# Optimization experiments

Hardware: AMD Instinct MI355X
Metric: run time of the kernel (lower is better)

The kernel has to match this reference:

```python
import jax, jax.numpy as jnp
import numpy as np

B, T, H, C = 32, 2048, 200, 256

def conv1d(x, w):
    # x: [B, T, Cin], w: [K, Cin, Cout], padding SAME, stride 1
    return jax.lax.conv_general_dilated(x, w, (1,), 'SAME',
                                        dimension_numbers=('NWC', 'WIO', 'NWC'))

def reverse_sequence(x, lengths):
    # tf.reverse_sequence along time axis 1
    t = jnp.arange(x.shape[1])[None, :]          # [1, T]
    L = lengths[:, None]                          # [B, 1]
    idx = jnp.where(t < L, L - 1 - t, t)          # [B, T]
    return jnp.take_along_axis(x, idx[:, :, None], axis=1)

def lstm(x, lengths, W, b):
    # BasicLSTMCell: gates [i, j, f, o], forget_bias=1.0
    xT = jnp.transpose(x, (1, 0, 2))              # [T, B, C]
    c0 = jnp.zeros((x.shape[0], H), x.dtype)
    h0 = jnp.zeros((x.shape[0], H), x.dtype)
    def step(carry, inp):
        c, h = carry
        xt, t = inp
        z = jnp.concatenate([xt, h], -1) @ W + b  # [B, 4H]
        i, j, f, o = jnp.split(z, 4, axis=-1)
        c_new = c * jax.nn.sigmoid(f + 1.0) + jax.nn.sigmoid(i) * jnp.tanh(j)
        h_new = jnp.tanh(c_new) * jax.nn.sigmoid(o)
        m = (t < lengths)[:, None]
        c2 = jnp.where(m, c_new, c)
        h2 = jnp.where(m, h_new, h)
        out = jnp.where(m, h_new, jnp.zeros_like(h_new))
        return (c2, h2), out
    _, ys = jax.lax.scan(step, (c0, h0), (xT, jnp.arange(xT.shape[0])))
    return jnp.transpose(ys, (1, 0, 2))           # [B, T, H]

def setup_inputs() -> dict:
    key = jax.random.key(0)
    ks = jax.random.split(key, 12)
    s = lambda k, shape, fan_in: jax.random.normal(k, shape, jnp.float32) * (1.0 / np.sqrt(fan_in))
    return {
        'signals': jax.random.normal(ks[0], (B, T, 1), jnp.float32),
        'sig_length': jax.random.randint(ks[1], (B,), T // 2, T + 1),
        'k1w': s(ks[2], (1, 1, C), 1),
        'k1aw': s(ks[3], (1, 1, C), 1),
        'k1ab': jnp.zeros((C,), jnp.float32),
        'k2w': s(ks[4], (3, C, C), 3 * C),
        'k3w': s(ks[5], (1, C, C), C),
        'Wf': s(ks[6], (C + H, 4 * H), C + H),
        'bf': jnp.zeros((4 * H,), jnp.float32),
        'Wb': s(ks[7], (C + H, 4 * H), C + H),
        'bb': jnp.zeros((4 * H,), jnp.float32),
        'Wd': s(ks[8], (2 * H, 5), 2 * H),
        'bd': jnp.zeros((5,), jnp.float32),
    }

def reference(signals, sig_length, k1w, k1aw, k1ab, k2w, k3w, Wf, bf, Wb, bb, Wd, bd):
    # resBlock
    conv1 = jax.nn.relu(conv1d(signals, k1w))
    conv1a = jax.nn.relu(conv1d(signals, k1aw) + k1ab)
    conv2 = jax.nn.relu(conv1d(conv1, k2w))
    conv3 = jax.nn.relu(conv1d(conv2, k3w))
    enc = conv3 + conv1a                               # [B, T, 256]
    # bidirectional LSTM
    fw = lstm(enc, sig_length, Wf, bf)                 # [B, T, 200]
    x_rev = reverse_sequence(enc, sig_length)
    bw = reverse_sequence(lstm(x_rev, sig_length, Wb, bb), sig_length)
    bi = jnp.concatenate([fw, bw], -1)                 # [B, T, 400]
    # dense decode to 5 logits (4 bases + blank)
    logits = bi @ Wd + bd                              # [B, T, 5]
    return logits
```

## Files before the change

### kernel.cpp

```cpp
#include <hip/hip_runtime.h>
#include <cstdint>

#define T_LEN 2048
#define NB    32
#define NROWS (NB*T_LEN)
#define HH    200
#define G4    800
#define TB    256
#define SB    8

typedef _Float16 f16;
typedef _Float16 f16x2 __attribute__((ext_vector_type(2)));
typedef _Float16 f16x8 __attribute__((ext_vector_type(8)));
typedef float   floatx4 __attribute__((ext_vector_type(4)));

#define GLD_LDS16(g, l) __builtin_amdgcn_global_load_lds( \
    (const __attribute__((address_space(1))) void*)(g), \
    (__attribute__((address_space(3))) void*)(l), 16, 0, 0)

static __device__ __forceinline__ unsigned short f2h(float x) {
  f16 h = (f16)x; return __builtin_bit_cast(unsigned short, h);
}
static __device__ __forceinline__ float dot2f(unsigned int a, unsigned int b, float c) {
  return __builtin_amdgcn_fdot2(__builtin_bit_cast(f16x2, a),
                                __builtin_bit_cast(f16x2, b), c, false);
}
static __device__ __forceinline__ float sigm(float x) {
  return __builtin_amdgcn_rcpf(1.f + __expf(-x));
}
static __device__ __forceinline__ float tanh_fast(float x) {
  return 1.f - 2.f * __builtin_amdgcn_rcpf(__expf(2.f * x) + 1.f);
}

__global__ void pq_kernel(const float* __restrict__ k1w, const float* __restrict__ k2w,
                          float* __restrict__ PQ) {
  int id = blockIdx.x * 256 + threadIdx.x;
  int pq = id / 768;
  int rem = id % 768;
  int wdt = rem / 256;
  int co  = rem % 256;
  float acc = 0.f;
  for (int ci = 0; ci < 256; ++ci) {
    float k = k1w[ci];
    float kk = pq ? fmaxf(-k, 0.f) : fmaxf(k, 0.f);
    acc += kk * k2w[((size_t)wdt * 256 + ci) * 256 + co];
  }
  PQ[id] = acc;
}

__global__ void prep_kernel(const float* __restrict__ k3w,
                            const float* __restrict__ Wf, const float* __restrict__ bfv,
                            const float* __restrict__ Wb, const float* __restrict__ bbv,
                            unsigned short* __restrict__ K3h, unsigned short* __restrict__ Wx2,
                            unsigned short* __restrict__ WhK, float* __restrict__ bcat) {
  int id = blockIdx.x * 256 + threadIdx.x;
  if (id < 65536) {
    K3h[id] = f2h(k3w[(id & 255) * 256 + (id >> 8)]);
    return;
  }
  id -= 65536;
  if (id < 409600) {
    int dirv = id / 204800;
    int r = id % 204800;
    int c = r >> 8, k = r & 255;
    int n = c >> 2, q = c & 3;
    int g = q * 200 + n;
    const float* W = dirv ? Wb : Wf;
    Wx2[id] = f2h(W[k * 800 + g]);
    return;
  }
  id -= 409600;
  if (id < 320000) {
    int rec = id / 160;
    int m   = id % 160;
    int g   = m / 40, j = m % 40;
    int n   = rec % 200;
    int t2  = rec / 200;
    int s   = t2 % 5, dirv = t2 / 5;
    int k   = s * 40 + j;
    const float* W = dirv ? Wb : Wf;
    WhK[id] = f2h(W[(256 + k) * 800 + (g * 200 + n)]);
    return;
  }
  id -= 320000;
  if (id < 1600) {
    int dirv = id / 800;
    int c = id % 800;
    int n = c >> 2, q = c & 3;
    int g = q * 200 + n;
    bcat[id] = (dirv ? bbv : bfv)[g] + (q == 2 ? 1.f : 0.f);
  }
}

__global__ void conv2_kernel(const float* __restrict__ s, const float* __restrict__ PQ,
                             unsigned short* __restrict__ C2) {
  int row = blockIdx.x;
  int co  = threadIdx.x;
  int t = row & (T_LEN - 1);
  float s0 = s[row];
  float sm = (t > 0)         ? s[row - 1] : 0.f;
  float sp = (t < T_LEN - 1) ? s[row + 1] : 0.f;
  const float* P = PQ;
  const float* Q = PQ + 768;
  float acc = 0.f;
  float a, m;
  a = fmaxf(sm, 0.f); m = fmaxf(-sm, 0.f);
  acc += a * P[0*256+co] + m * Q[0*256+co];
  a = fmaxf(s0, 0.f); m = fmaxf(-s0, 0.f);
  acc += a * P[1*256+co] + m * Q[1*256+co];
  a = fmaxf(sp, 0.f); m = fmaxf(-sp, 0.f);
  acc += a * P[2*256+co] + m * Q[2*256+co];
  C2[(size_t)row * 256 + co] = f2h(fmaxf(acc, 0.f));
}

__global__ __launch_bounds__(256, 2) void gemm_kernel(
    const unsigned short* __restrict__ Ag, const unsigned short* __restrict__ Bg0,
    int N, int ntiles, int mode,
    unsigned short* __restrict__ Outp,
    const float* __restrict__ bias, const float* __restrict__ Sg,
    const float* __restrict__ k1aw, const float* __restrict__ k1ab,
    const int* __restrict__ lens, int t0)
{
  __shared__ __align__(16) unsigned short Bl[128*128];
  __shared__ __align__(16) unsigned short Al[128*40];
  __shared__ int rowsrc[128];
  int tid = threadIdx.x;
  int tm = blockIdx.x / ntiles, tn = blockIdx.x % ntiles;
  int col0 = tn * 128;
  int lane = tid & 63, wv = tid >> 6;
  int quad = lane >> 4, l16 = lane & 15;
  int wrow = (wv & 1) * 64, wcol = (wv >> 1) * 64;

  int dirv = 0;
  if (mode == 2) dirv = ((tm * 128) >> 8) >> 5;
  const unsigned short* Bg = Bg0 + (size_t)dirv * 204800;

  if (tid < 128) {
    int r;
    if (mode == 2) {
      int m = tm * 128 + tid;
      int ch = m >> 8;
      int ls = m & 255;
      int b = ch & 31, dd = ch >> 5;
      int L = lens[b]; L = (L < 0) ? 0 : ((L > T_LEN) ? T_LEN : L);
      int t = t0 + ls;
      int src = dd ? (L - 1 - t) : t;
      src = (src < 0) ? 0 : ((src > T_LEN - 1) ? (T_LEN - 1) : src);
      r = b * T_LEN + src;
    } else {
      r = tm * 128 + tid;
    }
    rowsrc[tid] = r;
  }

  floatx4 acc[16];
  #pragma unroll
  for (int i = 0; i < 16; ++i) acc[i] = (floatx4){0.f,0.f,0.f,0.f};

  for (int ph = 0; ph < 2; ++ph) {
    __syncthreads();
    #pragma unroll
    for (int it = 0; it < 8; ++it) {
      int idx = it * 256 + tid;
      int n  = idx >> 4;
      int k8 = idx & 15;
      int nn = col0 + n;
      uint4 v = (uint4){0u,0u,0u,0u};
      if (nn < N) v = *(const uint4*)(Bg + (size_t)nn * 256 + ph * 128 + k8 * 8);
      *(uint4*)(&Bl[n * 128 + ((k8 ^ (n & 7)) * 8)]) = v;
    }
    for (int kb2 = 0; kb2 < 4; ++kb2) {
      int kb = ph * 4 + kb2;
      __syncthreads();
      #pragma unroll
      for (int i = 0; i < 2; ++i) {
        int c2 = i * 256 + tid;
        int r = c2 >> 2, kc = (c2 & 3) * 8;
        uint4 v = *(const uint4*)(Ag + (size_t)rowsrc[r] * 256 + kb * 32 + kc);
        *(uint4*)(&Al[r * 40 + kc]) = v;
      }
      __syncthreads();
      f16x8 af[4], bfr[4];
      #pragma unroll
      for (int mt = 0; mt < 4; ++mt)
        af[mt] = *(const f16x8*)(&Al[(wrow + mt*16 + l16) * 40 + quad * 8]);
      #pragma unroll
      for (int nt = 0; nt < 4; ++nt) {
        int nl = wcol + nt*16 + l16;
        int c = kb2 * 4 + quad;
        bfr[nt] = *(const f16x8*)(&Bl[nl * 128 + ((c ^ (nl & 7)) * 8)]);
      }
      #pragma unroll
      for (int mt = 0; mt < 4; ++mt)
        #pragma unroll
        for (int nt = 0; nt < 4; ++nt)
          acc[mt*4+nt] = __builtin_amdgcn_mfma_f32_16x16x32_f16(af[mt], bfr[nt], acc[mt*4+nt], 0, 0, 0);
    }
  }
  #pragma unroll
  for (int mt = 0; mt < 4; ++mt) {
    #pragma unroll
    for (int nt = 0; nt < 4; ++nt) {
      floatx4 v = acc[mt*4+nt];
      int col = col0 + wcol + nt*16 + l16;
      if (col < N) {
        #pragma unroll
        for (int r = 0; r < 4; ++r) {
          int row = tm * 128 + wrow + mt*16 + quad*4 + r;
          float x = v[r];
          float o;
          if (mode == 0) {
            float sv = Sg[row];
            float a1 = sv * k1aw[col] + k1ab[col];
            o = fmaxf(x, 0.f) + fmaxf(a1, 0.f);
          } else {
            o = x + bias[dirv * 800 + col];
          }
          Outp[(size_t)row * N + col] = f2h(o);
        }
      }
    }
  }
}

__global__ __launch_bounds__(1024, 4)
void lstm_kernel(
    const unsigned short* __restrict__ XWbuf,
    const unsigned short* __restrict__ WhK,
    const int* __restrict__ lens,
    unsigned short* __restrict__ fwH, unsigned short* __restrict__ bwH,
    float* __restrict__ cState, unsigned short* __restrict__ hState,
    int t0)
{
  int ch  = blockIdx.x;
  int dir = ch >> 5;
  int b   = ch & 31;
  int L = lens[b];
  L = (L < 0) ? 0 : ((L > T_LEN) ? T_LEN : L);
  int tend = t0 + TB; if (tend > L) tend = L;
  int tid = threadIdx.x;
  bool worker = tid < 1000;
  int s = tid / 200;
  int n = tid - s * 200;

  __shared__ __align__(16) unsigned short xw_lds[2][SB*800];
  __shared__ __align__(16) unsigned short hist[SB*200];
  __shared__ __align__(16) unsigned short himg[2][200];
  __shared__ __align__(16) floatx4 zp[800];

  if (tid < 200) ((unsigned int*)himg)[tid] = 0u;

  float c = 0.f;
  unsigned short last_h = 0;
  if (tid < 200 && t0 > 0) {
    c = cState[ch * HH + tid];
    last_h = hState[ch * HH + tid];
  }
  __syncthreads();
  if (tid < 200 && t0 > 0) himg[0][tid] = last_h;

  unsigned int w[80];
  if (worker) {
    const uint4* wp = (const uint4*)(WhK + ((size_t)((dir * 5 + s) * 200 + n)) * 160);
    #pragma unroll
    for (int r = 0; r < 20; ++r) {
      uint4 v = wp[r];
      w[4*r+0] = v.x; w[4*r+1] = v.y; w[4*r+2] = v.z; w[4*r+3] = v.w;
    }
    #pragma unroll
    for (int r = 0; r < 80; ++r)
      asm volatile("" : "+v"(w[r]));
  }

  unsigned short* Hd = dir ? bwH : fwH;
  const unsigned short* XWc = XWbuf + ((size_t)ch * TB) * 800;

  if (t0 < tend && tid < 800)
    GLD_LDS16(XWc + (size_t)tid * 8, &xw_lds[0][tid * 8]);
  __syncthreads();

  int buf = 0, cur = 0;
  int prev_tb = -1, prev_cnt = 0;

  for (int tb = t0; tb < tend; tb += SB) {
    int cnt = tend - tb; if (cnt > SB) cnt = SB;
    for (int sl = 0; sl < cnt; ++sl) {
      if (sl == 0) {
        int ntb = tb + SB;
        if ((ntb - t0) < TB && tid < 800) {
          const unsigned short* src = XWc + (size_t)(ntb - t0) * 800;
          GLD_LDS16(src + (size_t)tid * 8, &xw_lds[buf ^ 1][tid * 8]);
        }
        if (prev_tb >= 0) {
          int pcnt = prev_cnt;
          if (tid < pcnt * 25) {
            int srow = dir ? (pcnt - 1 - tid / 25) : (tid / 25);
            uint4 v = *(const uint4*)&hist[srow*200 + (tid % 25)*8];
            size_t base = dir ? ((size_t)(b*T_LEN + (L - prev_tb - pcnt)))*HH
                              : ((size_t)(b*T_LEN + prev_tb))*HH;
            *(uint4*)(Hd + base + (size_t)tid*8) = v;
          }
        }
      }
      float a0 = 0.f, a1 = 0.f, a2 = 0.f, a3 = 0.f;
      if (worker) {
        const uint4* hp = (const uint4*)(&himg[cur][s * 40]);
        #pragma unroll
        for (int r = 0; r < 5; ++r) {
          uint4 hv = hp[r];
          int d = r * 4;
          a0 = dot2f(hv.x, w[d],      a0); a1 = dot2f(hv.x, w[20 + d], a1);
          a2 = dot2f(hv.x, w[40 + d], a2); a3 = dot2f(hv.x, w[60 + d], a3);
          a0 = dot2f(hv.y, w[d + 1],  a0); a1 = dot2f(hv.y, w[21 + d], a1);
          a2 = dot2f(hv.y, w[41 + d], a2); a3 = dot2f(hv.y, w[61 + d], a3);
          a0 = dot2f(hv.z, w[d + 2],  a0); a1 = dot2f(hv.z, w[22 + d], a1);
          a2 = dot2f(hv.z, w[42 + d], a2); a3 = dot2f(hv.z, w[62 + d], a3);
          a0 = dot2f(hv.w, w[d + 3],  a0); a1 = dot2f(hv.w, w[23 + d], a1);
          a2 = dot2f(hv.w, w[43 + d], a2); a3 = dot2f(hv.w, w[63 + d], a3);
        }
        if (s != 0) {
          floatx4 z; z[0] = a0; z[1] = a1; z[2] = a2; z[3] = a3;
          zp[(s - 1) * 200 + n] = z;
        }
      }
      __syncthreads();
      if (tid < 200) {
        floatx4 p0 = zp[tid], p1 = zp[200 + tid], p2 = zp[400 + tid], p3 = zp[600 + tid];
        uint2 xv = *(const uint2*)&xw_lds[buf][sl*800 + 4*tid];
        f16x2 xa = __builtin_bit_cast(f16x2, xv.x);
        f16x2 xb = __builtin_bit_cast(f16x2, xv.y);
        float zi = a0 + p0[0] + p1[0] + p2[0] + p3[0] + (float)xa[0];
        float zj = a1 + p0[1] + p1[1] + p2[1] + p3[1] + (float)xa[1];
        float zf = a2 + p0[2] + p1[2] + p2[2] + p3[2] + (float)xb[0];
        float zo = a3 + p0[3] + p1[3] + p2[3] + p3[3] + (float)xb[1];
        c = c * sigm(zf) + sigm(zi) * tanh_fast(zj);
        float h = tanh_fast(c) * sigm(zo);
        unsigned short hh = f2h(h);
        last_h = hh;
        himg[cur ^ 1][tid] = hh;
        hist[sl*200 + tid] = hh;
      }
      cur ^= 1;
      __syncthreads();
    }
    prev_tb = tb; prev_cnt = cnt; buf ^= 1;
  }
  if (prev_tb >= 0) {
    int pcnt = prev_cnt;
    if (tid < pcnt * 25) {
      int srow = dir ? (pcnt - 1 - tid / 25) : (tid / 25);
      uint4 v = *(const uint4*)&hist[srow*200 + (tid % 25)*8];
      size_t base = dir ? ((size_t)(b*T_LEN + (L - prev_tb - pcnt)))*HH
                        : ((size_t)(b*T_LEN + prev_tb))*HH;
      *(uint4*)(Hd + base + (size_t)tid*8) = v;
    }
  }
  if (tid < 200) {
    cState[ch * HH + tid] = c;
    hState[ch * HH + tid] = last_h;
  }
}

__global__ __launch_bounds__(256) void out_kernel(
    const unsigned short* __restrict__ fwH, const unsigned short* __restrict__ bwH,
    const float* __restrict__ Wd, const float* __restrict__ bd, float* __restrict__ out)
{
  __shared__ float wd[2000];
  int tid = threadIdx.x;
  for (int i = tid; i < 2000; i += 256) wd[i] = Wd[i];
  __syncthreads();
  int row = blockIdx.x * 256 + tid;
  float acc0 = bd[0], acc1 = bd[1], acc2 = bd[2], acc3 = bd[3], acc4 = bd[4];
  const unsigned int* fu = (const unsigned int*)(fwH + (size_t)row * HH);
  const unsigned int* bu = (const unsigned int*)(bwH + (size_t)row * HH);
  #pragma unroll 4
  for (int i = 0; i < 100; ++i) {
    f16x2 pf = __builtin_bit_cast(f16x2, fu[i]);
    f16x2 pb = __builtin_bit_cast(f16x2, bu[i]);
    int k = 2 * i;
    float f0 = (float)pf[0], f1 = (float)pf[1];
    float b0 = (float)pb[0], b1 = (float)pb[1];
    const float* w0 = &wd[k*5];
    const float* w1 = &wd[(k+1)*5];
    const float* w2 = &wd[(200+k)*5];
    const float* w3 = &wd[(201+k)*5];
    acc0 += f0*w0[0] + f1*w1[0] + b0*w2[0] + b1*w3[0];
    acc1 += f0*w0[1] + f1*w1[1] + b0*w2[1] + b1*w3[1];
    acc2 += f0*w0[2] + f1*w1[2] + b0*w2[2] + b1*w3[2];
    acc3 += f0*w0[3] + f1*w1[3] + b0*w2[3] + b1*w3[3];
    acc4 += f0*w0[4] + f1*w1[4] + b0*w2[4] + b1*w3[4];
  }
  float* o = out + (size_t)row * 5;
  o[0]=acc0; o[1]=acc1; o[2]=acc2; o[3]=acc3; o[4]=acc4;
}

extern "C" void kernel_launch(void* const* d_in, const int* in_sizes, int n_in,
                              void* d_out, int out_size, void* d_ws, size_t ws_size,
                              hipStream_t stream)
{
  const float* signals = (const float*)d_in[0];
  const int*   lens    = (const int*)  d_in[1];
  const float* k1w     = (const float*)d_in[2];
  const float* k1aw    = (const float*)d_in[3];
  const float* k1ab    = (const float*)d_in[4];
  const float* k2w     = (const float*)d_in[5];
  const float* k3w     = (const float*)d_in[6];
  const float* Wf      = (const float*)d_in[7];
  const float* bf      = (const float*)d_in[8];
  const float* Wb      = (const float*)d_in[9];
  const float* bb      = (const float*)d_in[10];
  const float* Wd      = (const float*)d_in[11];
  const float* bd      = (const float*)d_in[12];
  float* out = (float*)d_out;
  char* ws = (char*)d_ws;

  size_t szC2   = (size_t)NROWS * 256 * 2;
  size_t szXWb  = (size_t)64 * TB * 800 * 2;
  size_t szA    = (szC2 > szXWb) ? szC2 : szXWb;
  size_t oA   = 0;
  size_t oE   = oA   + szA;
  size_t oFw  = oE   + (size_t)NROWS*256*2;
  size_t oBw  = oFw  + (size_t)NROWS*HH*2;
  size_t oWhK = oBw  + (size_t)NROWS*HH*2;
  size_t oWx2 = oWhK + (size_t)320000*2;
  size_t oK3  = oWx2 + (size_t)2*256*800*2;
  size_t oPQ  = oK3  + (size_t)256*256*2;
  size_t oBc  = oPQ  + 1536*4;
  size_t oCst = oBc  + 1600*4;
  size_t oHst = oCst + (size_t)64*HH*4;
  size_t total= oHst + (size_t)64*HH*2;
  if (ws_size < total) return;

  unsigned short* C2    = (unsigned short*)(ws + oA);
  unsigned short* XWbuf = (unsigned short*)(ws + oA);
  unsigned short* E     = (unsigned short*)(ws + oE);
  unsigned short* fwH   = (unsigned short*)(ws + oFw);
  unsigned short* bwH   = (unsigned short*)(ws + oBw);
  unsigned short* WhK   = (unsigned short*)(ws + oWhK);
  unsigned short* Wx2   = (unsigned short*)(ws + oWx2);
  unsigned short* K3h   = (unsigned short*)(ws + oK3);
  float* PQ     = (float*)(ws + oPQ);
  float* bcat   = (float*)(ws + oBc);
  float* cState = (float*)(ws + oCst);
  unsigned short* hState = (unsigned short*)(ws + oHst);

  (void)hipMemsetAsync(fwH, 0, (size_t)2*NROWS*HH*2, stream);
  pq_kernel  <<<6,     256, 0, stream>>>(k1w, k2w, PQ);
  prep_kernel<<<3113,  256, 0, stream>>>(k3w, Wf, bf, Wb, bb, K3h, Wx2, WhK, bcat);
  conv2_kernel<<<NROWS, 256, 0, stream>>>(signals, PQ, C2);
  gemm_kernel<<<1024,  256, 0, stream>>>(C2, K3h, 256, 2, 0, E, nullptr, signals, k1aw, k1ab, nullptr, 0);
  for (int t0 = 0; t0 < T_LEN; t0 += TB) {
    gemm_kernel<<<896, 256, 0, stream>>>(E, Wx2, 800, 7, 2, XWbuf, bcat, nullptr, nullptr, nullptr, lens, t0);
    lstm_kernel<<<64, 1024, 0, stream>>>(XWbuf, WhK, lens, fwH, bwH, cState, hState, t0);
  }
  out_kernel <<<256,   256, 0, stream>>>(fwH, bwH, Wd, bd, out);
}
```

Baseline: 2.573 ms.

## Overlap next chunk's input projection GEMM with LSTM recurrence in one kernel

Merges the per-chunk input-projection GEMM and the LSTM recurrence into a single launch. Blocks 0-63 run the recurrence for chunk k, while the remaining 150 blocks compute the XW projection for chunk k+1 into a second, double-buffered XW region. The time chunk is halved to 128 so the pipeline has more stages and fewer idle CUs. The cost is extra LDS per block from merging both kernels' shared buffers, which lowers occupancy. The GEMM now runs as 1024-thread blocks with only 256 threads active, and there are twice as many sequential launches.

```diff
diff --git a/kernel.cpp b/kernel.cpp
--- a/kernel.cpp
+++ b/kernel.cpp
@@ -6,8 +6,9 @@
 #define NROWS (NB*T_LEN)
 #define HH    200
 #define G4    800
-#define TB    256
+#define TB    128
 #define SB    8
+#define XWSZ  ((size_t)64 * TB * 800)
 
 typedef _Float16 f16;
 typedef _Float16 f16x2 __attribute__((ext_vector_type(2)));
@@ -132,15 +133,15 @@
   int wrow = (wv & 1) * 64, wcol = (wv >> 1) * 64;
 
   int dirv = 0;
-  if (mode == 2) dirv = ((tm * 128) >> 8) >> 5;
+  if (mode == 2) dirv = tm >> 5;
   const unsigned short* Bg = Bg0 + (size_t)dirv * 204800;
 
   if (tid < 128) {
     int r;
     if (mode == 2) {
       int m = tm * 128 + tid;
-      int ch = m >> 8;
-      int ls = m & 255;
+      int ch = m >> 7;
+      int ls = m & 127;
       int b = ch & 31, dd = ch >> 5;
       int L = lens[b]; L = (L < 0) ? 0 : ((L > T_LEN) ? T_LEN : L);
       int t = t0 + ls;
@@ -224,140 +225,246 @@
 }
 
 __global__ __launch_bounds__(1024, 4)
-void lstm_kernel(
-    const unsigned short* __restrict__ XWbuf,
+void mega_kernel(
+    const unsigned short* __restrict__ Eg,
+    const unsigned short* __restrict__ Wx2,
+    unsigned short* __restrict__ XWbuf,
+    const float* __restrict__ bcat,
     const unsigned short* __restrict__ WhK,
     const int* __restrict__ lens,
     unsigned short* __restrict__ fwH, unsigned short* __restrict__ bwH,
     float* __restrict__ cState, unsigned short* __restrict__ hState,
-    int t0)
+    int k)
 {
-  int ch  = blockIdx.x;
-  int dir = ch >> 5;
-  int b   = ch & 31;
-  int L = lens[b];
-  L = (L < 0) ? 0 : ((L > T_LEN) ? T_LEN : L);
-  int tend = t0 + TB; if (tend > L) tend = L;
-  int tid = threadIdx.x;
-  bool worker = tid < 1000;
-  int s = tid / 200;
-  int n = tid - s * 200;
-
   __shared__ __align__(16) unsigned short xw_lds[2][SB*800];
   __shared__ __align__(16) unsigned short hist[SB*200];
   __shared__ __align__(16) unsigned short himg[2][200];
   __shared__ __align__(16) floatx4 zp[800];
-
-  if (tid < 200) ((unsigned int*)himg)[tid] = 0u;
-
-  float c = 0.f;
-  unsigned short last_h = 0;
-  if (tid < 200 && t0 > 0) {
-    c = cState[ch * HH + tid];
-    last_h = hState[ch * HH + tid];
-  }
-  __syncthreads();
-  if (tid < 200 && t0 > 0) himg[0][tid] = last_h;
-
-  unsigned int w[80];
-  if (worker) {
-    const uint4* wp = (const uint4*)(WhK + ((size_t)((dir * 5 + s) * 200 + n)) * 160);
+  __shared__ __align__(16) unsigned short Bl[128*128];
+  __shared__ __align__(16) unsigned short Al[128*40];
+  __shared__ int rowsrc[128];
+
+  int tid = threadIdx.x;
+  int t0 = k * TB;
+
+  if (blockIdx.x < 64) {
+    int ch  = blockIdx.x;
+    int dir = ch >> 5;
+    int b   = ch & 31;
+    int L = lens[b];
+    L = (L < 0) ? 0 : ((L > T_LEN) ? T_LEN : L);
+    int tend = t0 + TB; if (tend > L) tend = L;
+    bool worker = tid < 1000;
+    int s = tid / 200;
+    int n = tid - s * 200;
+
+    if (tid < 200) ((unsigned int*)himg)[tid] = 0u;
+
+    float c = 0.f;
+    unsigned short last_h = 0;
+    if (tid < 200 && t0 > 0) {
+      c = cState[ch * HH + tid];
+      last_h = hState[ch * HH + tid];
+    }
+    __syncthreads();
+    if (tid < 200 && t0 > 0) himg[0][tid] = last_h;
+
+    unsigned int w[80];
+    if (worker) {
+      const uint4* wp = (const uint4*)(WhK + ((size_t)((dir * 5 + s) * 200 + n)) * 160);
+      #pragma unroll
+      for (int r = 0; r < 20; ++r) {
+        uint4 v = wp[r];
+        w[4*r+0] = v.x; w[4*r+1] = v.y; w[4*r+2] = v.z; w[4*r+3] = v.w;
+      }
+      #pragma unroll
+      for (int r = 0; r < 80; ++r)
+        asm volatile("" : "+v"(w[r]));
+    }
+
+    unsigned short* Hd = dir ? bwH : fwH;
+    const unsigned short* XWc = XWbuf + (size_t)(k & 1) * XWSZ + ((size_t)ch * TB) * 800;
+
+    if (t0 < tend && tid < 800)
+      GLD_LDS16(XWc + (size_t)tid * 8, &xw_lds[0][tid * 8]);
+    __syncthreads();
+
+    int buf = 0, cur = 0;
+    int prev_tb = -1, prev_cnt = 0;
+
+    for (int tb = t0; tb < tend; tb += SB) {
+      int cnt = tend - tb; if (cnt > SB) cnt = SB;
+      for (int sl = 0; sl < cnt; ++sl) {
+        if (sl == 0) {
+          int ntb = tb + SB;
+          if ((ntb - t0) < TB && tid < 800) {
+            const unsigned short* src = XWc + (size_t)(ntb - t0) * 800;
+            GLD_LDS16(src + (size_t)tid * 8, &xw_lds[buf ^ 1][tid * 8]);
+          }
+          if (prev_tb >= 0) {
+            int pcnt = prev_cnt;
+            if (tid < pcnt * 25) {
+              int srow = dir ? (pcnt - 1 - tid / 25) : (tid / 25);
+              uint4 v = *(const uint4*)&hist[srow*200 + (tid % 25)*8];
+              size_t base = dir ? ((size_t)(b*T_LEN + (L - prev_tb - pcnt)))*HH
+                                : ((size_t)(b*T_LEN + prev_tb))*HH;
+              *(uint4*)(Hd + base + (size_t)tid*8) = v;
+            }
+          }
+        }
+        float a0 = 0.f, a1 = 0.f, a2 = 0.f, a3 = 0.f;
+        if (worker) {
+          const uint4* hp = (const uint4*)(&himg[cur][s * 40]);
+          #pragma unroll
+          for (int r = 0; r < 5; ++r) {
+            uint4 hv = hp[r];
+            int d = r * 4;
+            a0 = dot2f(hv.x, w[d],      a0); a1 = dot2f(hv.x, w[20 + d], a1);
+            a2 = dot2f(hv.x, w[40 + d], a2); a3 = dot2f(hv.x, w[60 + d], a3);
+            a0 = dot2f(hv.y, w[d + 1],  a0); a1 = dot2f(hv.y, w[21 + d], a1);
+            a2 = dot2f(hv.y, w[41 + d], a2); a3 = dot2f(hv.y, w[61 + d], a3);
+            a0 = dot2f(hv.z, w[d + 2],  a0); a1 = dot2f(hv.z, w[22 + d], a1);
+            a2 = dot2f(hv.z, w[42 + d], a2); a3 = dot2f(hv.z, w[62 + d], a3);
+            a0 = dot2f(hv.w, w[d + 3],  a0); a1 = dot2f(hv.w, w[23 + d], a1);
+            a2 = dot2f(hv.w, w[43 + d], a2); a3 = dot2f(hv.w, w[63 + d], a3);
+          }
+          if (s != 0) {
+            floatx4 z; z[0] = a0; z[1] = a1; z[2] = a2; z[3] = a3;
+            zp[(s - 1) * 200 + n] = z;
+          }
+        }
+        __syncthreads();
+        if (tid < 200) {
+          floatx4 p0 = zp[tid], p1 = zp[200 + tid], p2 = zp[400 + tid], p3 = zp[600 + tid];
+          uint2 xv = *(const uint2*)&xw_lds[buf][sl*800 + 4*tid];
+          f16x2 xa = __builtin_bit_cast(f16x2, xv.x);
+          f16x2 xb = __builtin_bit_cast(f16x2, xv.y);
+          float zi = a0 + p0[0] + p1[0] + p2[0] + p3[0] + (float)xa[0];
+          float zj = a1 + p0[1] + p1[1] + p2[1] + p3[1] + (float)xa[1];
+          float zf = a2 + p0[2] + p1[2] + p2[2] + p3[2] + (float)xb[0];
+          float zo = a3 + p0[3] + p1[3] + p2[3] + p3[3] + (float)xb[1];
+          c = c * sigm(zf) + sigm(zi) * tanh_fast(zj);
+          float h = tanh_fast(c) * sigm(zo);
+          unsigned short hh = f2h(h);
+          last_h = hh;
+          himg[cur ^ 1][tid] = hh;
+          hist[sl*200 + tid] = hh;
+        }
+        cur ^= 1;
+        __syncthreads();
+      }
+      prev_tb = tb; prev_cnt = cnt; buf ^= 1;
+    }
+    if (prev_tb >= 0) {
+      int pcnt = prev_cnt;
+      if (tid < pcnt * 25) {
+        int srow = dir ? (pcnt - 1 - tid / 25) : (tid / 25);
+        uint4 v = *(const uint4*)&hist[srow*200 + (tid % 25)*8];
+        size_t base = dir ? ((size_t)(b*T_LEN + (L - prev_tb - pcnt)))*HH
+                          : ((size_t)(b*T_LEN + prev_tb))*HH;
+        *(uint4*)(Hd + base + (size_t)tid*8) = v;
+      }
+    }
+    if (tid < 200) {
+      cState[ch * HH + tid] = c;
+      hState[ch * HH + tid] = last_h;
+    }
+    return;
+  }
+
+  int tgem = t0 + TB;
+  if (tgem >= T_LEN) return;
+  unsigned short* Outp = XWbuf + (size_t)((k + 1) & 1) * XWSZ;
+  int lane = tid & 63, wv = tid >> 6;
+  int quad = lane >> 4, l16 = lane & 15;
+  int wrow = (wv & 1) * 64, wcol = (wv >> 1) * 64;
+
+  for (int task = blockIdx.x - 64; task < 448; task += 150) {
+    int tm = task / 7, tn = task % 7;
+    int col0 = tn * 128;
+    int dirv = tm >> 5;
+    const unsigned short* Bg = Wx2 + (size_t)dirv * 204800;
+
+    __syncthreads();
+    if (tid < 128) {
+      int m = tm * 128 + tid;
+      int chn = m >> 7;
+      int ls = m & 127;
+      int bb = chn & 31, dd = chn >> 5;
+      int L = lens[bb]; L = (L < 0) ? 0 : ((L > T_LEN) ? T_LEN : L);
+      int t = tgem + ls;
+      int src = dd ? (L - 1 - t) : t;
+      src = (src < 0) ? 0 : ((src > T_LEN - 1) ? (T_LEN - 1) : src);
+      rowsrc[tid] = bb * T_LEN + src;
+    }
+
+    floatx4 acc[16];
     #pragma unroll
-    for (int r = 0; r < 20; ++r) {
-      uint4 v = wp[r];
-      w[4*r+0] = v.x; w[4*r+1] = v.y; w[4*r+2] = v.z; w[4*r+3] = v.w;
-    }
-    #pragma unroll
-    for (int r = 0; r < 80; ++r)
-      asm volatile("" : "+v"(w[r]));
-  }
-
-  unsigned short* Hd = dir ? bwH : fwH;
-  const unsigned short* XWc = XWbuf + ((size_t)ch * TB) * 800;
-
-  if (t0 < tend && tid < 800)
-    GLD_LDS16(XWc + (size_t)tid * 8, &xw_lds[0][tid * 8]);
-  __syncthreads();
-
-  int buf = 0, cur = 0;
-  int prev_tb = -1, prev_cnt = 0;
-
-  for (int tb = t0; tb < tend; tb += SB) {
-    int cnt = tend - tb; if (cnt > SB) cnt = SB;
-    for (int sl = 0; sl < cnt; ++sl) {
-      if (sl == 0) {
-        int ntb = tb + SB;
-        if ((ntb - t0) < TB && tid < 800) {
-          const unsigned short* src = XWc + (size_t)(ntb - t0) * 800;
-          GLD_LDS16(src + (size_t)tid * 8, &xw_lds[buf ^ 1][tid * 8]);
-        }
-        if (prev_tb >= 0) {
-          int pcnt = prev_cnt;
-          if (tid < pcnt * 25) {
-            int srow = dir ? (pcnt - 1 - tid / 25) : (tid / 25);
-            uint4 v = *(const uint4*)&hist[srow*200 + (tid % 25)*8];
-            size_t base = dir ? ((size_t)(b*T_LEN + (L - prev_tb - pcnt)))*HH
-                              : ((size_t)(b*T_LEN + prev_tb))*HH;
-            *(uint4*)(Hd + base + (size_t)tid*8) = v;
-          }
-        }
-      }
-      float a0 = 0.f, a1 = 0.f, a2 = 0.f, a3 = 0.f;
-      if (worker) {
-        const uint4* hp = (const uint4*)(&himg[cur][s * 40]);
+    for (int i = 0; i < 16; ++i) acc[i] = (floatx4){0.f,0.f,0.f,0.f};
+
+    for (int ph = 0; ph < 2; ++ph) {
+      __syncthreads();
+      if (tid < 256) {
         #pragma unroll
-        for (int r = 0; r < 5; ++r) {
-          uint4 hv = hp[r];
-          int d = r * 4;
-          a0 = dot2f(hv.x, w[d],      a0); a1 = dot2f(hv.x, w[20 + d], a1);
-          a2 = dot2f(hv.x, w[40 + d], a2); a3 = dot2f(hv.x, w[60 + d], a3);
-          a0 = dot2f(hv.y, w[d + 1],  a0); a1 = dot2f(hv.y, w[21 + d], a1);
-          a2 = dot2f(hv.y, w[41 + d], a2); a3 = dot2f(hv.y, w[61 + d], a3);
-          a0 = dot2f(hv.z, w[d + 2],  a0); a1 = dot2f(hv.z, w[22 + d], a1);
-          a2 = dot2f(hv.z, w[42 + d], a2); a3 = dot2f(hv.z, w[62 + d], a3);
-          a0 = dot2f(hv.w, w[d + 3],  a0); a1 = dot2f(hv.w, w[23 + d], a1);
-          a2 = dot2f(hv.w, w[43 + d], a2); a3 = dot2f(hv.w, w[63 + d], a3);
-        }
-        if (s != 0) {
-          floatx4 z; z[0] = a0; z[1] = a1; z[2] = a2; z[3] = a3;
-          zp[(s - 1) * 200 + n] = z;
-        }
-      }
-      __syncthreads();
-      if (tid < 200) {
-        floatx4 p0 = zp[tid], p1 = zp[200 + tid], p2 = zp[400 + tid], p3 = zp[600 + tid];
-        uint2 xv = *(const uint2*)&xw_lds[buf][sl*800 + 4*tid];
-        f16x2 xa = __builtin_bit_cast(f16x2, xv.x);
-        f16x2 xb = __builtin_bit_cast(f16x2, xv.y);
-        float zi = a0 + p0[0] + p1[0] + p2[0] + p3[0] + (float)xa[0];
-        float zj = a1 + p0[1] + p1[1] + p2[1] + p3[1] + (float)xa[1];
-        float zf = a2 + p0[2] + p1[2] + p2[2] + p3[2] + (float)xb[0];
-        float zo = a3 + p0[3] + p1[3] + p2[3] + p3[3] + (float)xb[1];
-        c = c * sigm(zf) + sigm(zi) * tanh_fast(zj);
-        float h = tanh_fast(c) * sigm(zo);
-        unsigned short hh = f2h(h);
-        last_h = hh;
-        himg[cur ^ 1][tid] = hh;
-        hist[sl*200 + tid] = hh;
-      }
-      cur ^= 1;
-      __syncthreads();
-    }
-    prev_tb = tb; prev_cnt = cnt; buf ^= 1;
-  }
-  if (prev_tb >= 0) {
-    int pcnt = prev_cnt;
-    if (tid < pcnt * 25) {
-      int srow = dir ? (pcnt - 1 - tid / 25) : (tid / 25);
-      uint4 v = *(const uint4*)&hist[srow*200 + (tid % 25)*8];
-      size_t base = dir ? ((size_t)(b*T_LEN + (L - prev_tb - pcnt)))*HH
-                        : ((size_t)(b*T_LEN + prev_tb))*HH;
-      *(uint4*)(Hd + base + (size_t)tid*8) = v;
-    }
-  }
-  if (tid < 200) {
-    cState[ch * HH + tid] = c;
-    hState[ch * HH + tid] = last_h;
+        for (int it = 0; it < 8; ++it) {
+          int idx = it * 256 + tid;
+          int nl = idx >> 4;
+          int k8 = idx & 15;
+          int nn = col0 + nl;
+          uint4 v = (uint4){0u,0u,0u,0u};
+          if (nn < 800) v = *(const uint4*)(Bg + (size_t)nn * 256 + ph * 128 + k8 * 8);
+          *(uint4*)(&Bl[nl * 128 + ((k8 ^ (nl & 7)) * 8)]) = v;
+        }
+      }
+      for (int kb2 = 0; kb2 < 4; ++kb2) {
+        int kb = ph * 4 + kb2;
+        __syncthreads();
+        if (tid < 256) {
+          #pragma unroll
+          for (int i = 0; i < 2; ++i) {
+            int c2 = i * 256 + tid;
+            int r = c2 >> 2, kc = (c2 & 3) * 8;
+            uint4 v = *(const uint4*)(Eg + (size_t)rowsrc[r] * 256 + kb * 32 + kc);
+            *(uint4*)(&Al[r * 40 + kc]) = v;
+          }
+        }
+        __syncthreads();
+        if (tid < 256) {
+          f16x8 af[4], bfr[4];
+          #pragma unroll
+          for (int mt = 0; mt < 4; ++mt)
+            af[mt] = *(const f16x8*)(&Al[(wrow + mt*16 + l16) * 40 + quad * 8]);
+          #pragma unroll
+          for (int nt = 0; nt < 4; ++nt) {
+            int nl = wcol + nt*16 + l16;
+            int cx = kb2 * 4 + quad;
+            bfr[nt] = *(const f16x8*)(&Bl[nl * 128 + ((cx ^ (nl & 7)) * 8)]);
+          }
+          #pragma unroll
+          for (int mt = 0; mt < 4; ++mt)
+            #pragma unroll
+            for (int nt = 0; nt < 4; ++nt)
+              acc[mt*4+nt] = __builtin_amdgcn_mfma_f32_16x16x32_f16(af[mt], bfr[nt], acc[mt*4+nt], 0, 0, 0);
+        }
+      }
+    }
+    if (tid < 256) {
+      #pragma unroll
+      for (int mt = 0; mt < 4; ++mt) {
+        #pragma unroll
+        for (int nt = 0; nt < 4; ++nt) {
+          floatx4 v = acc[mt*4+nt];
+          int col = col0 + wcol + nt*16 + l16;
+          if (col < 800) {
+            #pragma unroll
+            for (int r = 0; r < 4; ++r) {
+              int row = tm * 128 + wrow + mt*16 + quad*4 + r;
+              Outp[(size_t)row * 800 + col] = f2h(v[r] + bcat[dirv * 800 + col]);
+            }
+          }
+        }
+      }
+    }
   }
 }
 
@@ -415,7 +522,7 @@
   char* ws = (char*)d_ws;
 
   size_t szC2   = (size_t)NROWS * 256 * 2;
-  size_t szXWb  = (size_t)64 * TB * 800 * 2;
+  size_t szXWb  = 2 * XWSZ * 2;
   size_t szA    = (szC2 > szXWb) ? szC2 : szXWb;
   size_t oA   = 0;
   size_t oE   = oA   + szA;
@@ -449,9 +556,9 @@
   prep_kernel<<<3113,  256, 0, stream>>>(k3w, Wf, bf, Wb, bb, K3h, Wx2, WhK, bcat);
   conv2_kernel<<<NROWS, 256, 0, stream>>>(signals, PQ, C2);
   gemm_kernel<<<1024,  256, 0, stream>>>(C2, K3h, 256, 2, 0, E, nullptr, signals, k1aw, k1ab, nullptr, 0);
-  for (int t0 = 0; t0 < T_LEN; t0 += TB) {
-    gemm_kernel<<<896, 256, 0, stream>>>(E, Wx2, 800, 7, 2, XWbuf, bcat, nullptr, nullptr, nullptr, lens, t0);
-    lstm_kernel<<<64, 1024, 0, stream>>>(XWbuf, WhK, lens, fwH, bwH, cState, hState, t0);
+  gemm_kernel<<<448,   256, 0, stream>>>(E, Wx2, 800, 7, 2, XWbuf, bcat, nullptr, nullptr, nullptr, lens, 0);
+  for (int k = 0; k < T_LEN / TB; ++k) {
+    mega_kernel<<<214, 1024, 0, stream>>>(E, Wx2, XWbuf, bcat, WhK, lens, fwH, bwH, cState, hState, k);
   }
   out_kernel <<<256,   256, 0, stream>>>(fwH, bwH, Wd, bd, out);
 }
```

Measured after the change: 2.347 ms. 1.1x faster.
